# Kernel tuning notes

Measured on AMD Instinct MI355X. Metric: run time of the kernel, lower is better.

## Reference

```python
import jax, jax.numpy as jnp
import numpy as np

DIM = 1024
HEADS = 16
HEAD_DIM = DIM // HEADS


def setup_inputs() -> dict:
    key = jax.random.key(0)
    ks = jax.random.split(key, 9)
    s = 1.0 / np.sqrt(DIM)
    return {
        "x": jax.random.normal(ks[0], (2, 2048, 1, DIM), dtype=jnp.float32),
        "Wq": jax.random.normal(ks[1], (DIM, DIM), dtype=jnp.float32) * s,
        "bq": jnp.zeros((DIM,), dtype=jnp.float32),
        "Wk": jax.random.normal(ks[2], (DIM, DIM), dtype=jnp.float32) * s,
        "bk": jnp.zeros((DIM,), dtype=jnp.float32),
        "Wv": jax.random.normal(ks[3], (DIM, DIM), dtype=jnp.float32) * s,
        "bv": jnp.zeros((DIM,), dtype=jnp.float32),
        "Wo": jax.random.normal(ks[4], (DIM, DIM), dtype=jnp.float32) * s,
        "bo": jnp.zeros((DIM,), dtype=jnp.float32),
    }


def reference(x, Wq, bq, Wk, bk, Wv, bv, Wo, bo):
    b, t, _, d = x.shape
    h, hd = HEADS, HEAD_DIM
    # torch Linear: y = x @ W.T + b
    q = (x @ Wq.T + bq).reshape(b, t, h, hd)
    k = (x @ Wk.T + bk).reshape(b, t, h, hd)
    v = (x @ Wv.T + bv).reshape(b, t, h, hd)
    # Source applies self.scaling (hd**-0.5) in torch AND divides by
    # sqrt(k_features) inside the jax chunk routine -> net scale 1/hd.
    q = q * (1.0 / hd)
    # key_chunk_size >= T -> one chunk; online softmax == exact stable softmax
    scores = jnp.einsum('bqhd,bkhd->bhqk', q, k)  # [B,H,T,T]
    w = jax.nn.softmax(scores, axis=-1)
    o = jnp.einsum('bhqk,bkhd->bqhd', w, v).reshape(b, t, d)
    return o @ Wo.T + bo
```

## Files before the change

kernel.cpp:

```cpp
#include <hip/hip_runtime.h>
#include <math.h>

typedef _Float16 f16;
typedef _Float16 f16x2 __attribute__((ext_vector_type(2)));
typedef _Float16 f16x4 __attribute__((ext_vector_type(4)));
typedef _Float16 f16x8 __attribute__((ext_vector_type(8)));
typedef float    f32x4 __attribute__((ext_vector_type(4)));

constexpr int DIM   = 1024;
constexpr int HEADS = 16;
constexpr int HD    = 64;
constexpr int BATCH = 2;
constexpr int SEQ   = 2048;
constexpr int MTOT  = BATCH * SEQ;
constexpr int NT2   = SEQ / 128;

#define QSCALE (1.4426950408889634f / 64.0f)

#define MFMA16(a, b, c) __builtin_amdgcn_mfma_f32_16x16x32_f16((a), (b), (c), 0, 0, 0)

__device__ __forceinline__ void glds16(const void* g, void* l) {
    __builtin_amdgcn_global_load_lds(
        (const __attribute__((address_space(1))) void*)g,
        (__attribute__((address_space(3))) void*)l, 16, 0, 0);
}

__device__ __forceinline__ float exp2_hw(float x) {
    float r;
    asm("v_exp_f32 %0, %1" : "=v"(r) : "v"(x));
    return r;
}

__device__ __forceinline__ f16x2 pk_f16(float a, float b) {
    return __builtin_bit_cast(f16x2, __builtin_amdgcn_cvt_pkrtz(a, b));
}

__global__ __launch_bounds__(256) void presplit_kernel(
    const float* __restrict__ x,  const float* __restrict__ Wq,
    const float* __restrict__ Wk, const float* __restrict__ Wv,
    const float* __restrict__ Wo,
    f16* __restrict__ Xh,  f16* __restrict__ WqH, f16* __restrict__ WkH,
    f16* __restrict__ WvH, f16* __restrict__ WoH)
{
    const int bid = blockIdx.x;
    const float* src; f16* dh; int row;
    if (bid < 4096)      { src = x;  dh = Xh;  row = bid; }
    else if (bid < 5120) { src = Wq; dh = WqH; row = bid - 4096; }
    else if (bid < 6144) { src = Wk; dh = WkH; row = bid - 5120; }
    else if (bid < 7168) { src = Wv; dh = WvH; row = bid - 6144; }
    else                 { src = Wo; dh = WoH; row = bid - 7168; }

    const int k = threadIdx.x * 4;
    const float4 v = *reinterpret_cast<const float4*>(&src[(size_t)row * DIM + k]);
    const int s = (row >> 1) & 3;
    const size_t o = (size_t)row * DIM + (k & ~31) + ((k & 31) ^ (s << 3));
    f16x4 h4;
    h4[0] = (f16)v.x; h4[1] = (f16)v.y; h4[2] = (f16)v.z; h4[3] = (f16)v.w;
    *reinterpret_cast<f16x4*>(&dh[o]) = h4;
}

template <int MODE>
__device__ __forceinline__ void gemm_plane_body(
    const f16* __restrict__ AhG, const f16* __restrict__ BhG,
    const float* __restrict__ bias, float* __restrict__ C,
    f16* __restrict__ F, float scale, f16* __restrict__ smem)
{
    const int tid = threadIdx.x;
    const int l   = tid & 63;
    const int w   = tid >> 6;
    const int wm  = (w >> 1) * 64;
    const int wn  = (w & 1) * 64;
    const int m0  = blockIdx.y * 128;
    const int n0  = blockIdx.x * 128;
    const int fr  = l & 15;
    const int fk  = (l >> 4) * 8;
    const int rg  = (l >> 4) * 4;
    const int fko = fk ^ (((fr >> 1) & 3) << 3);

    f32x4 acc[4][4] = {};

#define GSTAGE(B, K0) do {                                                  \
        _Pragma("unroll")                                                   \
        for (int j = 0; j < 4; ++j) {                                       \
            const int c = w * 4 + j;                             \
            const int p = c >> 3;                         \
            const f16* P = (p == 0) ? AhG : BhG;                            \
            const int r0 = (p == 0) ? m0 : n0;                              \
            const int row = r0 + (c & 7) * 16 + (l >> 2);                   \
            glds16(P + (size_t)row * DIM + (K0) + (l & 3) * 8,              \
                   smem + (B) * 8192 + c * 512);                            \
        }                                                                   \
    } while (0)

    GSTAGE(0, 0);
    int cur = 0;

    for (int k0 = 0; k0 < DIM; k0 += 32) {
        if (k0 + 32 < DIM) {
            GSTAGE(cur ^ 1, k0 + 32);
            asm volatile("s_waitcnt vmcnt(4)\ns_barrier" ::: "memory");
        } else {
            asm volatile("s_waitcnt vmcnt(0)\ns_barrier" ::: "memory");
        }

        const f16* Ah = smem + cur * 8192;
        const f16* Bh = Ah + 4096;

        f16x8 ah[4], bh[4];
        #pragma unroll
        for (int m = 0; m < 4; ++m)
            ah[m] = *reinterpret_cast<const f16x8*>(&Ah[(wm + m * 16 + fr) * 32 + fko]);
        #pragma unroll
        for (int n = 0; n < 4; ++n)
            bh[n] = *reinterpret_cast<const f16x8*>(&Bh[(wn + n * 16 + fr) * 32 + fko]);
        #pragma unroll
        for (int n = 0; n < 4; ++n)
            #pragma unroll
            for (int m = 0; m < 4; ++m) {
                if (MODE == 1)
                    acc[m][n] = MFMA16(bh[n], ah[m], acc[m][n]);
                else
                    acc[m][n] = MFMA16(ah[m], bh[n], acc[m][n]);
            }
        asm volatile("s_barrier" ::: "memory");
        cur ^= 1;
    }
#undef GSTAGE

    if (MODE == 0 || MODE == 3) {
        #pragma unroll
        for (int n = 0; n < 4; ++n) {
            const int col  = n0 + wn + n * 16 + fr;
            const float bb = bias[col];
            #pragma unroll
            for (int m = 0; m < 4; ++m) {
                #pragma unroll
                for (int r = 0; r < 4; ++r) {
                    const int row = m0 + wm + m * 16 + rg + r;
                    const float v = (acc[m][n][r] + bb) * scale;
                    if (MODE == 0) C[(size_t)row * DIM + col] = v;
                    else           F[(size_t)row * DIM + col] = (f16)v;
                }
            }
        }
    } else if (MODE == 1) {
        constexpr int RS = 72;
        const int batch = m0 >> 11;
        const int kvg0  = m0 & 2047;
        for (int s = 0; s < 2; ++s) {
            __syncthreads();
            if ((w & 1) == s) {
                #pragma unroll
                for (int n = 0; n < 4; ++n) {
                    #pragma unroll
                    for (int m = 0; m < 4; ++m) {
                        const int kvrow = wm + m * 16 + fr;
                        const int dd    = n * 16 + rg;
                        f16x4 h4;
                        #pragma unroll
                        for (int r = 0; r < 4; ++r)
                            h4[r] = (f16)(acc[m][n][r] + bias[n0 + wn + dd + r]);
                        const int o = kvrow * RS + (dd ^ ((kvrow & 7) << 3));
                        *reinterpret_cast<f16x4*>(&smem[o]) = h4;
                    }
                }
            }
            __syncthreads();
            const size_t bh_ = (size_t)batch * HEADS + (n0 >> 6) + s;
            const int row = tid >> 1, c0 = (tid & 1) * 32;
            #pragma unroll
            for (int j = 0; j < 4; ++j) {
                const int so = row * RS + c0 + j * 8;
                const size_t go = bh_ * 131072 + (size_t)(kvg0 + row) * 64 + c0 + j * 8;
                *reinterpret_cast<f16x8*>(&F[go]) =
                    *reinterpret_cast<const f16x8*>(&smem[so]);
            }
        }
    } else {
        constexpr int RS = 136;
        const int batch = m0 >> 11;
        const int kvg0  = m0 & 2047;
        for (int s = 0; s < 2; ++s) {
            __syncthreads();
            if ((w & 1) == s) {
                #pragma unroll
                for (int n = 0; n < 4; ++n) {
                    const int d    = n * 16 + fr;
                    const float bb = bias[n0 + wn + d];
                    #pragma unroll
                    for (int m = 0; m < 4; ++m) {
                        const int kvl = wm + m * 16 + rg;
                        f16x4 h4;
                        h4[0] = (f16)(acc[m][n][0] + bb);
                        h4[1] = (f16)(acc[m][n][1] + bb);
                        h4[2] = (f16)(acc[m][n][2] + bb);
                        h4[3] = (f16)(acc[m][n][3] + bb);
                        const int o = d * RS + (kvl ^ ((d & 7) << 3));
                        *reinterpret_cast<f16x4*>(&smem[o]) = h4;
                    }
                }
            }
            __syncthreads();
            const size_t bh_ = (size_t)batch * HEADS + (n0 >> 6) + s;
            const int row = tid >> 2, c0 = (tid & 3) * 32;
            #pragma unroll
            for (int j = 0; j < 4; ++j) {
                const int so = row * RS + c0 + j * 8;
                const size_t go = bh_ * 131072 + (size_t)row * 2048 + kvg0 + c0 + j * 8;
                *reinterpret_cast<f16x8*>(&F[go]) =
                    *reinterpret_cast<const f16x8*>(&smem[so]);
            }
        }
    }
}

__global__ __launch_bounds__(256) void qkv_kernel(
    const f16* __restrict__ XhG,
    const f16* __restrict__ WqH, const float* __restrict__ bq,
    const f16* __restrict__ WkH, const float* __restrict__ bk,
    const f16* __restrict__ WvH, const float* __restrict__ bv,
    f16* __restrict__ QhG, f16* __restrict__ KhG, f16* __restrict__ VhG)
{
    __shared__ __align__(16) f16 smem[18432];
    if (blockIdx.z == 0)
        gemm_plane_body<3>(XhG, WqH, bq, nullptr, QhG, QSCALE, smem);
    else if (blockIdx.z == 1)
        gemm_plane_body<1>(XhG, WkH, bk, nullptr, KhG, 1.0f, smem);
    else
        gemm_plane_body<2>(XhG, WvH, bv, nullptr, VhG, 1.0f, smem);
}

__global__ __launch_bounds__(256) void oproj_kernel(
    const f16* __restrict__ OhG, const f16* __restrict__ WoH,
    const float* __restrict__ bo, float* __restrict__ out)
{
    __shared__ __align__(16) f16 smem[16384];
    gemm_plane_body<0>(OhG, WoH, bo, out, nullptr, 1.0f, smem);
}

__global__ __launch_bounds__(256, 2) void attn_kernel(
    const f16* __restrict__ QhG, const f16* __restrict__ KhG,
    const f16* __restrict__ VhG, f16* __restrict__ OhG)
{
    __shared__ __align__(16) f16 lds[2][2][8192];
    __shared__ __align__(16) f16 PL[4][2][1024];

    const int tid = threadIdx.x;
    const int l   = tid & 63;
    const int w   = tid >> 6;
    const int fr  = l & 15;
    const int g   = l >> 4;
    const int fk  = g * 8;
    const int rg  = g * 4;
    const int swz = (fr & 7) << 3;

    const int lin  = blockIdx.x + 16 * (blockIdx.y + 16 * blockIdx.z);
    const int sid  = (lin & 7) * 64 + (lin >> 3);
    const int qblk = sid & 15;
    const int head = (sid >> 4) & 15;
    const int batch = sid >> 8;

    const int q0 = qblk * 128;
    const size_t rowbase = (size_t)batch * SEQ;
    const int hcol = head * HD;
    const size_t bhbase = ((size_t)batch * HEADS + head) * (size_t)(SEQ * HD);

    size_t kA[4], vA[4];
    #pragma unroll
    for (int c = 0; c < 4; ++c) {
        const int h0 = (w * 4 + c) * 512 + l * 8;
        kA[c] = bhbase + (size_t)h0;
        vA[c] = bhbase + (size_t)(h0 >> 7) * 2048 + (h0 & 127);
    }

#define STAGE(B, T) do {                                                    \
        const size_t _ko = (size_t)(T) * 8192;                              \
        const size_t _vo = (size_t)(T) * 128;                               \
        _Pragma("unroll")                                                   \
        for (int c = 0; c < 4; ++c) {                                       \
            const int lo_ = (w * 4 + c) * 512;                              \
            glds16(KhG + kA[c] + _ko, &lds[B][0][lo_]);                     \
            glds16(VhG + vA[c] + _vo, &lds[B][1][lo_]);                     \
        }                                                                   \
    } while (0)

    STAGE(0, 0);

    f16x8 qh[2][2];
    #pragma unroll
    for (int qb = 0; qb < 2; ++qb) {
        const f16* qp = &QhG[(rowbase + q0 + w * 32 + qb * 16 + fr) * DIM + hcol];
        qh[qb][0] = *reinterpret_cast<const f16x8*>(&qp[fk]);
        qh[qb][1] = *reinterpret_cast<const f16x8*>(&qp[32 + fk]);
    }

    f16x8 onesv;
    #pragma unroll
    for (int i = 0; i < 8; ++i) onesv[i] = (f16)1.0f;

    f32x4 ls[2] = {};
    f32x4 oa[4][2] = {};

    int cur = 0;
    for (int t = 0; t < NT2; ++t) {
        asm volatile("s_waitcnt vmcnt(0) lgkmcnt(0)\ns_barrier" ::: "memory");
        if (t + 1 < NT2) STAGE(cur ^ 1, t + 1);

        #pragma unroll
        for (int hh = 0; hh < 2; ++hh) {
            const f16* Kh = &lds[cur][0][hh * 4096];
            const f16* Vh = &lds[cur][1][hh * 64];

            f32x4 sa[4][2] = {};
            __builtin_amdgcn_s_setprio(1);
            #pragma unroll
            for (int kvb = 0; kvb < 4; ++kvb) {
                #pragma unroll
                for (int ks = 0; ks < 2; ++ks) {
                    const int o = ((kvb * 16 + fr) * 64 + ks * 32 + fk) ^ swz;
                    const f16x8 kh = *reinterpret_cast<const f16x8*>(&Kh[o]);
                    sa[kvb][0] = MFMA16(kh, qh[0][ks], sa[kvb][0]);
                    sa[kvb][1] = MFMA16(kh, qh[1][ks], sa[kvb][1]);
                }
            }
            __builtin_amdgcn_s_setprio(0);

            f16x8 pf[2][2];
            #pragma unroll
            for (int qb = 0; qb < 2; ++qb) {
                f16* Wh = &PL[w][qb][0];
                #pragma unroll
                for (int kvb = 0; kvb < 4; ++kvb) {
                    const f16x2 p01 = pk_f16(exp2_hw(sa[kvb][qb][0]),
                                             exp2_hw(sa[kvb][qb][1]));
                    const f16x2 p23 = pk_f16(exp2_hw(sa[kvb][qb][2]),
                                             exp2_hw(sa[kvb][qb][3]));
                    f16x4 h4;
                    h4[0] = p01[0]; h4[1] = p01[1]; h4[2] = p23[0]; h4[3] = p23[1];
                    const int po = (fr * 64 + kvb * 16 + rg) ^ swz;
                    *reinterpret_cast<f16x4*>(&Wh[po]) = h4;
                }
                #pragma unroll
                for (int ks = 0; ks < 2; ++ks) {
                    const int ro = (fr * 64 + ks * 32 + fk) ^ swz;
                    pf[qb][ks] = *reinterpret_cast<const f16x8*>(&Wh[ro]);
                }
            }

            __builtin_amdgcn_s_setprio(1);
            #pragma unroll
            for (int qb = 0; qb < 2; ++qb)
                #pragma unroll
                for (int ks = 0; ks < 2; ++ks)
                    ls[qb] = MFMA16(onesv, pf[qb][ks], ls[qb]);
            #pragma unroll
            for (int db = 0; db < 4; ++db) {
                #pragma unroll
                for (int ks = 0; ks < 2; ++ks) {
                    const int vo = (db * 16 + fr) * 128 + ((ks * 32 + fk) ^ swz);
                    const f16x8 vh = *reinterpret_cast<const f16x8*>(&Vh[vo]);
                    oa[db][0] = MFMA16(vh, pf[0][ks], oa[db][0]);
                    oa[db][1] = MFMA16(vh, pf[1][ks], oa[db][1]);
                }
            }
            __builtin_amdgcn_s_setprio(0);
        }
        cur ^= 1;
    }
#undef STAGE

    #pragma unroll
    for (int qb = 0; qb < 2; ++qb) {
        const float inv = 1.0f / ls[qb][0];
        const size_t row = rowbase + q0 + w * 32 + qb * 16 + fr;
        const int s = ((int)row >> 1) & 3;
        #pragma unroll
        for (int db = 0; db < 4; ++db) {
            f16x4 h4;
            #pragma unroll
            for (int j = 0; j < 4; ++j) h4[j] = (f16)(oa[db][qb][j] * inv);
            const int kg = hcol + db * 16 + rg;
            const size_t o = row * DIM + (kg & ~31) + ((kg & 31) ^ (s << 3));
            *reinterpret_cast<f16x4*>(&OhG[o]) = h4;
        }
    }
}

extern "C" void kernel_launch(void* const* d_in, const int* in_sizes, int n_in,
                              void* d_out, int out_size, void* d_ws, size_t ws_size,
                              hipStream_t stream)
{
    const float* x  = (const float*)d_in[0];
    const float* Wq = (const float*)d_in[1];
    const float* bq = (const float*)d_in[2];
    const float* Wk = (const float*)d_in[3];
    const float* bk = (const float*)d_in[4];
    const float* Wv = (const float*)d_in[5];
    const float* bv = (const float*)d_in[6];
    const float* Wo = (const float*)d_in[7];
    const float* bo = (const float*)d_in[8];
    float* out = (float*)d_out;

    const size_t PS = (size_t)MTOT * DIM;
    f16* QhG = (f16*)d_ws;
    f16* KhG = QhG + PS;
    f16* VhG = KhG + PS;
    f16* XhG = VhG + PS;
    f16* WqH = XhG + PS;
    f16* WkH = WqH + (size_t)DIM * DIM;
    f16* WvH = WkH + (size_t)DIM * DIM;
    f16* WoH = WvH + (size_t)DIM * DIM;
    f16* OhG = XhG;

    presplit_kernel<<<8192, 256, 0, stream>>>(x, Wq, Wk, Wv, Wo,
                                              XhG, WqH, WkH, WvH, WoH);

    dim3 gqkv(DIM / 128, MTOT / 128, 3);
    qkv_kernel<<<gqkv, 256, 0, stream>>>(XhG, WqH, bq, WkH, bk, WvH, bv,
                                         QhG, KhG, VhG);

    dim3 gattn(SEQ / 128, HEADS, BATCH);
    attn_kernel<<<gattn, 256, 0, stream>>>(QhG, KhG, VhG, OhG);

    dim3 gout(DIM / 128, MTOT / 128);
    oproj_kernel<<<gout, 256, 0, stream>>>(OhG, WoH, bo, out);
}
```

Baseline: 115.9 us.

## Double attention query tile to 256 rows per block for K/V reuse

Each attention block now handles 256 query rows instead of 128, with each wave owning 64 rows (four 16-row subtiles). Every K/V tile staged in LDS is therefore reused across twice as many queries, which halves K/V global traffic and the number of staging barriers per query. The cost is higher register pressure, since the launch bound drops to one block per SIMD group, and a grid of only 256 blocks, which may underfill the GPU's compute units.

```diff
diff --git a/kernel.cpp b/kernel.cpp
--- a/kernel.cpp
+++ b/kernel.cpp
@@ -238,12 +238,12 @@
     gemm_plane_body<0>(OhG, WoH, bo, out, nullptr, 1.0f, smem);
 }
 
-__global__ __launch_bounds__(256, 2) void attn_kernel(
+__global__ __launch_bounds__(256, 1) void attn_kernel(
     const f16* __restrict__ QhG, const f16* __restrict__ KhG,
     const f16* __restrict__ VhG, f16* __restrict__ OhG)
 {
     __shared__ __align__(16) f16 lds[2][2][8192];
-    __shared__ __align__(16) f16 PL[4][2][1024];
+    __shared__ __align__(16) f16 PL[4][4][1024];
 
     const int tid = threadIdx.x;
     const int l   = tid & 63;
@@ -254,13 +254,13 @@
     const int rg  = g * 4;
     const int swz = (fr & 7) << 3;
 
-    const int lin  = blockIdx.x + 16 * (blockIdx.y + 16 * blockIdx.z);
-    const int sid  = (lin & 7) * 64 + (lin >> 3);
-    const int qblk = sid & 15;
-    const int head = (sid >> 4) & 15;
-    const int batch = sid >> 8;
-
-    const int q0 = qblk * 128;
+    const int lin  = blockIdx.x + 8 * (blockIdx.y + 16 * blockIdx.z);
+    const int sid  = (lin & 7) * 32 + (lin >> 3);
+    const int qblk = sid & 7;
+    const int head = (sid >> 3) & 15;
+    const int batch = sid >> 7;
+
+    const int q0 = qblk * 256;
     const size_t rowbase = (size_t)batch * SEQ;
     const int hcol = head * HD;
     const size_t bhbase = ((size_t)batch * HEADS + head) * (size_t)(SEQ * HD);
@@ -286,20 +286,20 @@
 
     STAGE(0, 0);
 
-    f16x8 qh[2][2];
+    f16x8 qh[4][2];
     #pragma unroll
-    for (int qb = 0; qb < 2; ++qb) {
-        const f16* qp = &QhG[(rowbase + q0 + w * 32 + qb * 16 + fr) * DIM + hcol];
-        qh[qb][0] = *reinterpret_cast<const f16x8*>(&qp[fk]);
-        qh[qb][1] = *reinterpret_cast<const f16x8*>(&qp[32 + fk]);
+    for (int qs = 0; qs < 4; ++qs) {
+        const f16* qp = &QhG[(rowbase + q0 + w * 64 + qs * 16 + fr) * DIM + hcol];
+        qh[qs][0] = *reinterpret_cast<const f16x8*>(&qp[fk]);
+        qh[qs][1] = *reinterpret_cast<const f16x8*>(&qp[32 + fk]);
     }
 
     f16x8 onesv;
     #pragma unroll
     for (int i = 0; i < 8; ++i) onesv[i] = (f16)1.0f;
 
-    f32x4 ls[2] = {};
-    f32x4 oa[4][2] = {};
+    f32x4 ls[4] = {};
+    f32x4 oa[4][4] = {};
 
     int cur = 0;
     for (int t = 0; t < NT2; ++t) {
@@ -311,7 +311,7 @@
             const f16* Kh = &lds[cur][0][hh * 4096];
             const f16* Vh = &lds[cur][1][hh * 64];
 
-            f32x4 sa[4][2] = {};
+            f32x4 sa[4][4] = {};
             __builtin_amdgcn_s_setprio(1);
             #pragma unroll
             for (int kvb = 0; kvb < 4; ++kvb) {
@@ -319,22 +319,23 @@
                 for (int ks = 0; ks < 2; ++ks) {
                     const int o = ((kvb * 16 + fr) * 64 + ks * 32 + fk) ^ swz;
                     const f16x8 kh = *reinterpret_cast<const f16x8*>(&Kh[o]);
-                    sa[kvb][0] = MFMA16(kh, qh[0][ks], sa[kvb][0]);
-                    sa[kvb][1] = MFMA16(kh, qh[1][ks], sa[kvb][1]);
+                    #pragma unroll
+                    for (int qs = 0; qs < 4; ++qs)
+                        sa[kvb][qs] = MFMA16(kh, qh[qs][ks], sa[kvb][qs]);
                 }
             }
             __builtin_amdgcn_s_setprio(0);
 
-            f16x8 pf[2][2];
-            #pragma unroll
-            for (int qb = 0; qb < 2; ++qb) {
-                f16* Wh = &PL[w][qb][0];
+            f16x8 pf[4][2];
+            #pragma unroll
+            for (int qs = 0; qs < 4; ++qs) {
+                f16* Wh = &PL[w][qs][0];
                 #pragma unroll
                 for (int kvb = 0; kvb < 4; ++kvb) {
-                    const f16x2 p01 = pk_f16(exp2_hw(sa[kvb][qb][0]),
-                                             exp2_hw(sa[kvb][qb][1]));
-                    const f16x2 p23 = pk_f16(exp2_hw(sa[kvb][qb][2]),
-                                             exp2_hw(sa[kvb][qb][3]));
+                    const f16x2 p01 = pk_f16(exp2_hw(sa[kvb][qs][0]),
+                                             exp2_hw(sa[kvb][qs][1]));
+                    const f16x2 p23 = pk_f16(exp2_hw(sa[kvb][qs][2]),
+                                             exp2_hw(sa[kvb][qs][3]));
                     f16x4 h4;
                     h4[0] = p01[0]; h4[1] = p01[1]; h4[2] = p23[0]; h4[3] = p23[1];
                     const int po = (fr * 64 + kvb * 16 + rg) ^ swz;
@@ -343,24 +344,25 @@
                 #pragma unroll
                 for (int ks = 0; ks < 2; ++ks) {
                     const int ro = (fr * 64 + ks * 32 + fk) ^ swz;
-                    pf[qb][ks] = *reinterpret_cast<const f16x8*>(&Wh[ro]);
+                    pf[qs][ks] = *reinterpret_cast<const f16x8*>(&Wh[ro]);
                 }
             }
 
             __builtin_amdgcn_s_setprio(1);
             #pragma unroll
-            for (int qb = 0; qb < 2; ++qb)
+            for (int qs = 0; qs < 4; ++qs)
                 #pragma unroll
                 for (int ks = 0; ks < 2; ++ks)
-                    ls[qb] = MFMA16(onesv, pf[qb][ks], ls[qb]);
+                    ls[qs] = MFMA16(onesv, pf[qs][ks], ls[qs]);
             #pragma unroll
             for (int db = 0; db < 4; ++db) {
                 #pragma unroll
                 for (int ks = 0; ks < 2; ++ks) {
                     const int vo = (db * 16 + fr) * 128 + ((ks * 32 + fk) ^ swz);
                     const f16x8 vh = *reinterpret_cast<const f16x8*>(&Vh[vo]);
-                    oa[db][0] = MFMA16(vh, pf[0][ks], oa[db][0]);
-                    oa[db][1] = MFMA16(vh, pf[1][ks], oa[db][1]);
+                    #pragma unroll
+                    for (int qs = 0; qs < 4; ++qs)
+                        oa[db][qs] = MFMA16(vh, pf[qs][ks], oa[db][qs]);
                 }
             }
             __builtin_amdgcn_s_setprio(0);
@@ -370,15 +372,15 @@
 #undef STAGE
 
     #pragma unroll
-    for (int qb = 0; qb < 2; ++qb) {
-        const float inv = 1.0f / ls[qb][0];
-        const size_t row = rowbase + q0 + w * 32 + qb * 16 + fr;
+    for (int qs = 0; qs < 4; ++qs) {
+        const float inv = 1.0f / ls[qs][0];
+        const size_t row = rowbase + q0 + w * 64 + qs * 16 + fr;
         const int s = ((int)row >> 1) & 3;
         #pragma unroll
         for (int db = 0; db < 4; ++db) {
             f16x4 h4;
             #pragma unroll
-            for (int j = 0; j < 4; ++j) h4[j] = (f16)(oa[db][qb][j] * inv);
+            for (int j = 0; j < 4; ++j) h4[j] = (f16)(oa[db][qs][j] * inv);
             const int kg = hcol + db * 16 + rg;
             const size_t o = row * DIM + (kg & ~31) + ((kg & 31) ^ (s << 3));
             *reinterpret_cast<f16x4*>(&OhG[o]) = h4;
@@ -419,7 +421,7 @@
     qkv_kernel<<<gqkv, 256, 0, stream>>>(XhG, WqH, bq, WkH, bk, WvH, bv,
                                          QhG, KhG, VhG);
 
-    dim3 gattn(SEQ / 128, HEADS, BATCH);
+    dim3 gattn(SEQ / 256, HEADS, BATCH);
     attn_kernel<<<gattn, 256, 0, stream>>>(QhG, KhG, VhG, OhG);
 
     dim3 gout(DIM / 128, MTOT / 128);
```

Measured after the change: 125.5 us. 8.3% more time.
